# Optimization experiments

Hardware: AMD Instinct MI355X
Metric: run time of the kernel (lower is better)

## Reference

```python
import jax, jax.numpy as jnp
import numpy as np

N, E, H = 5000, 40000, 8
DIMS = [(258, 512), (516, 256), (262, 128), (136, 20)]  # (in_feature, out_feature) per GATDeformer


def setup_inputs() -> dict:
    key = jax.random.key(0)
    ks = jax.random.split(key, 10)
    s = 0.05
    data = jax.random.normal(ks[0], (N, 10), jnp.float32)
    src = jax.random.randint(ks[1], (E,), 0, N)
    off = jax.random.randint(ks[2], (E,), 1, N)
    edge_idx = jnp.stack([src, (src + off) % N]).astype(jnp.int32)  # no self loops by construction
    inp = {
        'data': data,
        'edge_idx': edge_idx,
        'W0': jax.random.normal(ks[3], (10, 256), jnp.float32) * s,
        'b0': jnp.zeros((256,), jnp.float32),
    }
    for i, (din, dout) in enumerate(DIMS, start=1):
        k = jax.random.split(ks[3 + i], 3)
        inp[f'W{i}'] = jax.random.normal(k[0], (din, H * dout), jnp.float32) * s
        inp[f'asrc{i}'] = jax.random.normal(k[1], (H, dout), jnp.float32) * s
        inp[f'adst{i}'] = jax.random.normal(k[2], (H, dout), jnp.float32) * s
        inp[f'bias{i}'] = jnp.zeros((dout,), jnp.float32)
    return inp


def _gat(x, src, dst, W, a_s, a_d, b):
    """PyG GATConv (concat=False): returns (mean-over-heads output + bias, alpha [E',H])."""
    Hh, C = a_s.shape
    h = (x @ W).reshape(N, Hh, C)                               # [N,H,C]
    e_s = jnp.einsum('nhc,hc->nh', h, a_s)                      # [N,H]
    e_d = jnp.einsum('nhc,hc->nh', h, a_d)
    logits = jax.nn.leaky_relu(e_s[src] + e_d[dst], 0.2)        # [E',H]
    m = jax.ops.segment_max(logits, dst, num_segments=N)        # segment softmax over incoming edges
    ex = jnp.exp(logits - m[dst])
    alpha = ex / jax.ops.segment_sum(ex, dst, num_segments=N)[dst]
    out = jax.ops.segment_sum(alpha[:, :, None] * h[src], dst, num_segments=N)  # [N,H,C]
    return out.mean(axis=1) + b, alpha


def _deformer(af, src, dst, W, a_s, a_d, b):
    # find_boundary on the layer input features
    up, down = af[:, 0] == 1.0, af[:, 0] == 0.0
    left, right = af[:, 1] == 0.0, af[:, 1] == 1.0
    feat, alpha = _gat(af, src, dst, W, a_s, a_d, b)
    coord = af[:, :2]
    # second propagate: alpha*0.2 reused to aggregate source coordinates, then mean over heads
    msg = (alpha * 0.2)[:, :, None] * coord[src][:, None, :]    # [E',H,2]
    oc = jax.ops.segment_sum(msg, dst, num_segments=N).mean(axis=1)
    # fix_boundary (sequential overwrite order: up then down, left then right)
    c0 = jnp.where(down, 0.0, jnp.where(up, 1.0, oc[:, 0]))
    c1 = jnp.where(right, 1.0, jnp.where(left, 0.0, oc[:, 1]))
    return jnp.stack([c0, c1], axis=1), jax.nn.selu(feat)


def reference(data, edge_idx, W0, b0, W1, asrc1, adst1, bias1, W2, asrc2, adst2, bias2, W3, asrc3, adst3, bias3, W4, asrc4, adst4, bias4):
    sl = jnp.arange(N, dtype=edge_idx.dtype)
    src = jnp.concatenate([edge_idx[0], sl])   # GATConv add_self_loops=True
    dst = jnp.concatenate([edge_idx[1], sl])
    coord = data[:, :2]
    feat = jax.nn.selu(data @ W0 + b0)
    c1_, f1 = _deformer(jnp.concatenate([coord, feat], 1), src, dst, W1, asrc1, adst1, bias1)
    c2_, f2 = _deformer(jnp.concatenate([c1_, coord, f1], 1), src, dst, W2, asrc2, adst2, bias2)
    c3_, f3 = _deformer(jnp.concatenate([c2_, c1_, coord, f2], 1), src, dst, W3, asrc3, adst3, bias3)
    c4_, _ = _deformer(jnp.concatenate([c3_, c2_, c1_, coord, f3], 1), src, dst, W4, asrc4, adst4, bias4)
    return c4_
```

## Files before the change

### kernel.cpp

```cpp
#include <hip/hip_runtime.h>

#define N_NODES 5000
#define NH 8

typedef unsigned short u16;
typedef short bf16x8 __attribute__((ext_vector_type(8)));
typedef float f32x4 __attribute__((ext_vector_type(4)));

static __device__ __forceinline__ float selu_f(float x) {
    const float sc = 1.0507009873554805f;
    const float al = 1.6732632423543772f;
    return x > 0.f ? sc * x : sc * al * (__expf(x) - 1.f);
}

static __device__ __forceinline__ u16 f2bf(float x) {
    union { float f; unsigned u; } v; v.f = x;
    unsigned r = v.u + 0x7fff + ((v.u >> 16) & 1);
    return (u16)(r >> 16);
}

static __device__ __forceinline__ float bf2f(unsigned hi16) {
    union { unsigned u; float f; } v; v.u = hi16 << 16;
    return v.f;
}

#define GL2LDS16(gp, lp)                                                        \
    __builtin_amdgcn_global_load_lds(                                           \
        (const __attribute__((address_space(1))) void*)(gp),                    \
        (__attribute__((address_space(3))) void*)(lp), 16, 0, 0)

__global__ void k_count(const int* __restrict__ ei, int* cnt, int E, int Esz) {
    int e = blockIdx.x * 256 + threadIdx.x;
    if (e >= Esz) return;
    int dst = (e < E) ? ei[E + e] : (e - E);
    atomicAdd(&cnt[dst], 1);
}

__global__ void k_scan(const int* __restrict__ cnt, int* __restrict__ rowp, int n) {
    __shared__ int ps[256];
    int t = threadIdx.x;
    int per = (n + 255) / 256;
    int b = t * per;
    int s = 0;
    for (int i = 0; i < per; ++i) { int idx = b + i; if (idx < n) s += cnt[idx]; }
    ps[t] = s;
    __syncthreads();
    for (int off = 1; off < 256; off <<= 1) {
        int v = (t >= off) ? ps[t - off] : 0;
        __syncthreads();
        ps[t] += v;
        __syncthreads();
    }
    int run = (t == 0) ? 0 : ps[t - 1];
    for (int i = 0; i < per; ++i) {
        int idx = b + i;
        if (idx < n) { rowp[idx] = run; run += cnt[idx]; }
    }
    if (t == 255) rowp[n] = run;
}

__global__ void k_fill(const int* __restrict__ ei, const int* __restrict__ rowp,
                       int* cur, int* ssrc, int E, int Esz) {
    int e = blockIdx.x * 256 + threadIdx.x;
    if (e >= Esz) return;
    int src, dst;
    if (e < E) { src = ei[e]; dst = ei[E + e]; }
    else       { src = e - E; dst = src; }
    int pos = rowp[dst] + atomicAdd(&cur[dst], 1);
    ssrc[pos] = src;
}

__global__ __launch_bounds__(256) void k_prep(
        const float* W1, const float* W2, const float* W3, const float* W4,
        const float* s1, const float* s2, const float* s3, const float* s4,
        const float* d1, const float* d2, const float* d3, const float* d4,
        float* __restrict__ fsAll, float* __restrict__ fdAll,
        u16* T1, u16* T2, u16* T3) {
    const int Ks[4] = {258, 516, 262, 136};
    const int Cs[4] = {512, 256, 128, 20};
    int bid = blockIdx.x;
    if (bid < 516) {
        int li = bid / 129;
        int k = (bid % 129) * 4 + (threadIdx.x >> 6);
        int lane = threadIdx.x & 63;
        if (k >= Ks[li]) return;
        const float* W  = (li == 0) ? W1 : (li == 1) ? W2 : (li == 2) ? W3 : W4;
        const float* as = (li == 0) ? s1 : (li == 1) ? s2 : (li == 2) ? s3 : s4;
        const float* ad = (li == 0) ? d1 : (li == 1) ? d2 : (li == 2) ? d3 : d4;
        int C = Cs[li];
        float s[8] = {0.f,0.f,0.f,0.f,0.f,0.f,0.f,0.f};
        float d[8] = {0.f,0.f,0.f,0.f,0.f,0.f,0.f,0.f};
        const float* wr = W + (size_t)k * 8 * C;
        for (int c = lane; c < C; c += 64) {
            #pragma unroll
            for (int h = 0; h < 8; ++h) {
                float w = wr[h * C + c];
                s[h] += w * as[h * C + c];
                d[h] += w * ad[h * C + c];
            }
        }
        #pragma unroll
        for (int off = 32; off >= 1; off >>= 1) {
            #pragma unroll
            for (int h = 0; h < 8; ++h) {
                s[h] += __shfl_xor(s[h], off);
                d[h] += __shfl_xor(d[h], off);
            }
        }
        if (lane == 0) {
            float* fo = fsAll + (size_t)li * 516 * 8 + k * 8;
            float* go = fdAll + (size_t)li * 516 * 8 + k * 8;
            #pragma unroll
            for (int h = 0; h < 8; ++h) { fo[h] = s[h]; go[h] = d[h]; }
        }
    } else {
        const int Kps[3] = {288, 544, 288};
        int w = bid - 516;
        int li = w / (16 * 136);
        int rem = w % (16 * 136);
        int c0 = (rem % 16) * 32;
        int j0 = (rem / 16) * 32;
        int C = Cs[li], K = Ks[li], Kp = Kps[li], KK = 8 * Kp;
        if (c0 >= C || j0 >= KK) return;
        const float* W = (li == 0) ? W1 : (li == 1) ? W2 : W3;
        u16* Wt2 = (li == 0) ? T1 : (li == 1) ? T2 : T3;
        __shared__ float tile[32][33];
        int h = j0 / Kp, k0 = j0 % Kp;
        int tid = threadIdx.x;
        for (int idx = tid; idx < 1024; idx += 256) {
            int kr = idx >> 5, cc = idx & 31;
            int gk = k0 + kr;
            tile[kr][cc] = (gk < K) ? W[(size_t)gk * (8 * C) + h * C + c0 + cc] : 0.f;
        }
        __syncthreads();
        for (int idx = tid; idx < 1024; idx += 256) {
            int cr = idx >> 5, kc = idx & 31;
            Wt2[(size_t)(c0 + cr) * KK + j0 + kc] = f2bf(tile[kc][cr]);
        }
    }
}

__global__ __launch_bounds__(256) void k_mf(const float* p0, const float* p1,
                                            const float* p2, const float* p3, int np,
                                            const float* __restrict__ data,
                                            const float* __restrict__ W0,
                                            const float* __restrict__ b0,
                                            const u16* __restrict__ facc,
                                            const float* __restrict__ biasp,
                                            int split, int MN, int FC, int K, int Kp,
                                            const float* __restrict__ fs,
                                            const float* __restrict__ fd,
                                            u16* __restrict__ afb,
                                            float* __restrict__ es, float* __restrict__ ed,
                                            float* __restrict__ c0out) {
    int n = blockIdx.x, t = threadIdx.x;
    __shared__ float drow[10];
    bool l1 = (biasp == nullptr);
    if (l1 && t < 10) drow[t] = data[n * 10 + t];
    __syncthreads();
    float pes[8] = {0.f,0.f,0.f,0.f,0.f,0.f,0.f,0.f};
    float ped[8] = {0.f,0.f,0.f,0.f,0.f,0.f,0.f,0.f};
    u16* rowb = afb + (size_t)n * Kp;
    for (int cf = t; cf < FC; cf += 256) {
        float v;
        if (l1) {
            v = b0[cf];
            #pragma unroll
            for (int k = 0; k < 10; ++k) v += drow[k] * W0[k * 256 + cf];
            v = selu_f(v);
        } else {
            float s = 0.f;
            for (int z = 0; z < split; ++z)
                s += bf2f(facc[(size_t)z * MN + (size_t)n * FC + cf]);
            v = selu_f(s * 0.125f + biasp[cf]);
        }
        int c = 2 * np + cf;
        rowb[c] = f2bf(v);
        const float* fsr = fs + c * 8;
        const float* fdr = fd + c * 8;
        #pragma unroll
        for (int h = 0; h < 8; ++h) { pes[h] += v * fsr[h]; ped[h] += v * fdr[h]; }
    }
    if (t < 2 * np) {
        float v;
        if (l1) {
            v = drow[t];
            c0out[n * 2 + t] = v;
        } else {
            const float* p = (t < 2) ? p0 : (t < 4) ? p1 : (t < 6) ? p2 : p3;
            v = p[n * 2 + (t & 1)];
        }
        rowb[t] = f2bf(v);
        #pragma unroll
        for (int h = 0; h < 8; ++h) { pes[h] += v * fs[t * 8 + h]; ped[h] += v * fd[t * 8 + h]; }
    }
    for (int c = K + t; c < Kp; c += 256) rowb[c] = 0;
    #pragma unroll
    for (int off = 32; off >= 1; off >>= 1) {
        #pragma unroll
        for (int h = 0; h < 8; ++h) {
            pes[h] += __shfl_xor(pes[h], off);
            ped[h] += __shfl_xor(ped[h], off);
        }
    }
    __shared__ float red[4][16];
    int wv = t >> 6, ln = t & 63;
    if (ln == 0) {
        #pragma unroll
        for (int h = 0; h < 8; ++h) { red[wv][h] = pes[h]; red[wv][8 + h] = ped[h]; }
    }
    __syncthreads();
    if (t < 16) {
        float s = red[0][t] + red[1][t] + red[2][t] + red[3][t];
        if (t < 8) es[n * 8 + t] = s;
        else       ed[n * 8 + (t - 8)] = s;
    }
}

template <int S32>
__global__ __launch_bounds__(256) void k_gag(const float* __restrict__ es,
                            const float* __restrict__ ed,
                            const int* __restrict__ rowp, const int* __restrict__ ssrc,
                            const float* __restrict__ cprev, const u16* __restrict__ afb,
                            u16* __restrict__ g, float* __restrict__ cnext, int Kp) {
    __shared__ int   ls[128];
    __shared__ float la[128 * 8];
    __shared__ float lc0[128], lc1[128], lw[128];
    __shared__ float linv[8];
    int n = blockIdx.x, t = threadIdx.x;
    int s0 = rowp[n];
    int deg = rowp[n + 1] - s0;
    if (deg > 128) deg = 128;
    for (int i = t; i < deg; i += 256) {
        int src = ssrc[s0 + i];
        ls[i] = src;
        lc0[i] = cprev[src * 2];
        lc1[i] = cprev[src * 2 + 1];
    }
    __syncthreads();
    for (int i = t; i < deg * 8; i += 256) {
        int e = i >> 3, h = i & 7;
        float x = es[ls[e] * 8 + h] + ed[n * 8 + h];
        la[i] = x > 0.f ? x : 0.2f * x;
    }
    __syncthreads();
    if (t < 8) {
        float m = -1e30f;
        for (int e = 0; e < deg; ++e) m = fmaxf(m, la[e * 8 + t]);
        float s = 0.f;
        for (int e = 0; e < deg; ++e) {
            float v = __expf(la[e * 8 + t] - m);
            la[e * 8 + t] = v;
            s += v;
        }
        linv[t] = 1.f / s;
    }
    __syncthreads();
    for (int i = t; i < deg; i += 256) {
        float w = 0.f;
        #pragma unroll
        for (int h = 0; h < 8; ++h) w += la[i * 8 + h] * linv[h];
        lw[i] = w;
    }
    int nW = Kp >> 1;
    float acc[8][2 * S32];
    #pragma unroll
    for (int h = 0; h < 8; ++h)
        #pragma unroll
        for (int s = 0; s < 2 * S32; ++s) acc[h][s] = 0.f;
    int e = 0;
    for (; e + 1 < deg; e += 2) {
        const unsigned* r0 = (const unsigned*)(afb + (size_t)ls[e] * Kp);
        const unsigned* r1 = (const unsigned*)(afb + (size_t)ls[e + 1] * Kp);
        unsigned v0[S32], v1[S32];
        #pragma unroll
        for (int s = 0; s < S32; ++s) {
            int w = t + 256 * s;
            v0[s] = (w < nW) ? r0[w] : 0u;
            v1[s] = (w < nW) ? r1[w] : 0u;
        }
        float a0[8], a1[8];
        #pragma unroll
        for (int h = 0; h < 8; ++h) { a0[h] = la[e * 8 + h]; a1[h] = la[(e + 1) * 8 + h]; }
        #pragma unroll
        for (int s = 0; s < S32; ++s) {
            float x0 = bf2f(v0[s] & 0xffff), y0 = bf2f(v0[s] >> 16);
            float x1 = bf2f(v1[s] & 0xffff), y1 = bf2f(v1[s] >> 16);
            #pragma unroll
            for (int h = 0; h < 8; ++h) {
                acc[h][2 * s]     += a0[h] * x0 + a1[h] * x1;
                acc[h][2 * s + 1] += a0[h] * y0 + a1[h] * y1;
            }
        }
    }
    if (e < deg) {
        const unsigned* r0 = (const unsigned*)(afb + (size_t)ls[e] * Kp);
        unsigned v0[S32];
        #pragma unroll
        for (int s = 0; s < S32; ++s) {
            int w = t + 256 * s;
            v0[s] = (w < nW) ? r0[w] : 0u;
        }
        float a0[8];
        #pragma unroll
        for (int h = 0; h < 8; ++h) a0[h] = la[e * 8 + h];
        #pragma unroll
        for (int s = 0; s < S32; ++s) {
            float x0 = bf2f(v0[s] & 0xffff), y0 = bf2f(v0[s] >> 16);
            #pragma unroll
            for (int h = 0; h < 8; ++h) {
                acc[h][2 * s]     += a0[h] * x0;
                acc[h][2 * s + 1] += a0[h] * y0;
            }
        }
    }
    unsigned* grw = (unsigned*)(g + (size_t)n * 8 * Kp);
    #pragma unroll
    for (int s = 0; s < S32; ++s) {
        int w = t + 256 * s;
        if (w < nW) {
            #pragma unroll
            for (int h = 0; h < 8; ++h) {
                float iv = linv[h];
                unsigned lo = f2bf(acc[h][2 * s] * iv);
                unsigned hi = f2bf(acc[h][2 * s + 1] * iv);
                grw[h * nW + w] = lo | (hi << 16);
            }
        }
    }
    __syncthreads();
    if (t == 0) {
        float oc0 = 0.f, oc1 = 0.f;
        for (int i = 0; i < deg; ++i) { oc0 += lw[i] * lc0[i]; oc1 += lw[i] * lc1[i]; }
        oc0 *= 0.025f; oc1 *= 0.025f;
        float a0 = cprev[n * 2], a1 = cprev[n * 2 + 1];
        cnext[n * 2]     = (a0 == 0.f) ? 0.f : ((a0 == 1.f) ? 1.f : oc0);
        cnext[n * 2 + 1] = (a1 == 1.f) ? 1.f : ((a1 == 0.f) ? 0.f : oc1);
    }
}

__global__ __launch_bounds__(256) void k_gemm_s(const u16* __restrict__ A,
                                                const u16* __restrict__ Bt,
                                                u16* __restrict__ facc16,
                                                int M, int KK, int NC, int kchunk, int MN) {
    __shared__ u16 As[128 * 32];
    __shared__ u16 Bs[128 * 32];
    int tid = threadIdx.x;
    int wave = tid >> 6, lane = tid & 63;
    int bm = blockIdx.y * 128, bn = blockIdx.x * 128, z = blockIdx.z;
    int kbeg = z * kchunk, kend = min(KK, kbeg + kchunk);
    int wm = (wave >> 1) * 64, wn = (wave & 1) * 64;
    int l16 = lane & 15, q = lane >> 4;
    f32x4 acc[4][4] = {};

    int seg0 = wave * 128 + lane;
    int seg1 = seg0 + 64;
    int row0 = seg0 >> 2, sq0 = (seg0 & 3) ^ (row0 & 3);
    int row1 = seg1 >> 2, sq1 = (seg1 & 3) ^ (row1 & 3);
    const u16* ga0 = A  + (size_t)(bm + row0) * KK + sq0 * 8;
    const u16* ga1 = A  + (size_t)(bm + row1) * KK + sq1 * 8;
    const u16* gb0 = Bt + (size_t)(bn + row0) * KK + sq0 * 8;
    const u16* gb1 = Bt + (size_t)(bn + row1) * KK + sq1 * 8;
    u16* lA0 = As + (wave * 2 + 0) * 512;
    u16* lA1 = As + (wave * 2 + 1) * 512;
    u16* lB0 = Bs + (wave * 2 + 0) * 512;
    u16* lB1 = Bs + (wave * 2 + 1) * 512;

    for (int k0 = kbeg; k0 < kend; k0 += 32) {
        GL2LDS16(ga0 + k0, lA0);
        GL2LDS16(ga1 + k0, lA1);
        GL2LDS16(gb0 + k0, lB0);
        GL2LDS16(gb1 + k0, lB1);
        __syncthreads();
        bf16x8 fa[4], fb[4];
        #pragma unroll
        for (int mi = 0; mi < 4; ++mi) {
            int row = wm + mi * 16 + l16;
            fa[mi] = *(const bf16x8*)(As + row * 32 + ((q ^ (row & 3)) * 8));
            int col = wn + mi * 16 + l16;
            fb[mi] = *(const bf16x8*)(Bs + col * 32 + ((q ^ (col & 3)) * 8));
        }
        #pragma unroll
        for (int mi = 0; mi < 4; ++mi)
            #pragma unroll
            for (int ni = 0; ni < 4; ++ni)
                acc[mi][ni] = __builtin_amdgcn_mfma_f32_16x16x32_bf16(fa[mi], fb[ni], acc[mi][ni], 0, 0, 0);
        __syncthreads();
    }
    u16* out = facc16 + (size_t)z * MN;
    #pragma unroll
    for (int mi = 0; mi < 4; ++mi) {
        int row0s = bm + wm + mi * 16 + q * 4;
        #pragma unroll
        for (int ni = 0; ni < 4; ++ni) {
            int col = bn + wn + ni * 16 + l16;
            #pragma unroll
            for (int r = 0; r < 4; ++r) {
                int row = row0s + r;
                if (row < M) out[(size_t)row * NC + col] = f2bf(acc[mi][ni][r]);
            }
        }
    }
}

__global__ void k_final(const float* __restrict__ es, const float* __restrict__ ed,
                        const int* __restrict__ rowp, const int* __restrict__ ssrc,
                        const float* __restrict__ cprev, float* __restrict__ outp) {
    int wid = (blockIdx.x * blockDim.x + threadIdx.x) >> 6;
    int lane = threadIdx.x & 63;
    if (wid >= N_NODES) return;
    int n = wid;
    int s0 = rowp[n], deg = rowp[n + 1] - s0;
    int h = lane & 7, ei = lane >> 3;
    float edh = ed[n * 8 + h];
    float m = -1e30f;
    for (int b = 0; b < deg; b += 8) {
        int e = b + ei;
        if (e < deg) {
            int src = ssrc[s0 + e];
            float x = es[src * 8 + h] + edh;
            x = x > 0.f ? x : 0.2f * x;
            m = fmaxf(m, x);
        }
    }
    m = fmaxf(m, __shfl_xor(m, 8));
    m = fmaxf(m, __shfl_xor(m, 16));
    m = fmaxf(m, __shfl_xor(m, 32));
    float ssum = 0.f;
    for (int b = 0; b < deg; b += 8) {
        int e = b + ei;
        if (e < deg) {
            int src = ssrc[s0 + e];
            float x = es[src * 8 + h] + edh;
            x = x > 0.f ? x : 0.2f * x;
            ssum += __expf(x - m);
        }
    }
    ssum += __shfl_xor(ssum, 8);
    ssum += __shfl_xor(ssum, 16);
    ssum += __shfl_xor(ssum, 32);
    float inv = 1.f / ssum;
    float oc0 = 0.f, oc1 = 0.f;
    for (int b = 0; b < deg; b += 8) {
        int e = b + ei;
        if (e < deg) {
            int src = ssrc[s0 + e];
            float x = es[src * 8 + h] + edh;
            x = x > 0.f ? x : 0.2f * x;
            float w = __expf(x - m) * inv;
            w += __shfl_xor(w, 1);
            w += __shfl_xor(w, 2);
            w += __shfl_xor(w, 4);
            if (h == 0) {
                oc0 += w * cprev[src * 2];
                oc1 += w * cprev[src * 2 + 1];
            }
        }
    }
    oc0 += __shfl_xor(oc0, 8);  oc1 += __shfl_xor(oc1, 8);
    oc0 += __shfl_xor(oc0, 16); oc1 += __shfl_xor(oc1, 16);
    oc0 += __shfl_xor(oc0, 32); oc1 += __shfl_xor(oc1, 32);
    if (lane == 0) {
        oc0 *= 0.025f; oc1 *= 0.025f;
        float a0 = cprev[n * 2], a1 = cprev[n * 2 + 1];
        outp[n * 2]     = (a0 == 0.f) ? 0.f : ((a0 == 1.f) ? 1.f : oc0);
        outp[n * 2 + 1] = (a1 == 1.f) ? 1.f : ((a1 == 0.f) ? 0.f : oc1);
    }
}

extern "C" void kernel_launch(void* const* d_in, const int* in_sizes, int n_in,
                              void* d_out, int out_size, void* d_ws, size_t ws_size,
                              hipStream_t stream) {
    const float* data = (const float*)d_in[0];
    const int* ei = (const int*)d_in[1];
    const float* W0 = (const float*)d_in[2];
    const float* b0 = (const float*)d_in[3];
    int E = in_sizes[1] / 2;
    int Esz = E + N_NODES;

    char* wp = (char*)d_ws;
    size_t off = 0;
    auto alloc = [&](size_t bytes) {
        void* p = wp + off;
        off += (bytes + 1023) & ~(size_t)1023;
        return p;
    };
    u16*   g     = (u16*)alloc((size_t)N_NODES * 8 * 576 * 2);
    u16*   T1    = (u16*)alloc((size_t)512 * 8 * 288 * 2);
    u16*   T2    = (u16*)alloc((size_t)256 * 8 * 544 * 2);
    u16*   T3    = (u16*)alloc((size_t)128 * 8 * 288 * 2);
    u16*   facc  = (u16*)alloc((size_t)8 * N_NODES * 512 * 2);
    u16*   afb   = (u16*)alloc((size_t)N_NODES * 576 * 2);
    float* es    = (float*)alloc((size_t)N_NODES * 8 * 4);
    float* ebd   = (float*)alloc((size_t)N_NODES * 8 * 4);
    float* fsAll = (float*)alloc((size_t)4 * 516 * 8 * 4);
    float* fdAll = (float*)alloc((size_t)4 * 516 * 8 * 4);
    float* c0    = (float*)alloc(N_NODES * 2 * 4);
    float* c1    = (float*)alloc(N_NODES * 2 * 4);
    float* c2    = (float*)alloc(N_NODES * 2 * 4);
    float* c3    = (float*)alloc(N_NODES * 2 * 4);
    int* cnt  = (int*)alloc(N_NODES * 2 * 4);
    int* cur  = cnt + N_NODES;
    int* rowp = (int*)alloc((N_NODES + 1) * 4);
    int* ssrc = (int*)alloc(Esz * 4);

    hipMemsetAsync(cnt, 0, N_NODES * 2 * 4, stream);
    int gE = (Esz + 255) / 256;
    k_count<<<gE, 256, 0, stream>>>(ei, cnt, E, Esz);
    k_scan<<<1, 256, 0, stream>>>(cnt, rowp, N_NODES);
    k_fill<<<gE, 256, 0, stream>>>(ei, rowp, cur, ssrc, E, Esz);

    struct LP { const float *W, *as, *ad, *bs; int K, C, split; };
    LP L[4] = {
        {(const float*)d_in[4],  (const float*)d_in[5],  (const float*)d_in[6],  (const float*)d_in[7],  258, 512, 4},
        {(const float*)d_in[8],  (const float*)d_in[9],  (const float*)d_in[10], (const float*)d_in[11], 516, 256, 8},
        {(const float*)d_in[12], (const float*)d_in[13], (const float*)d_in[14], (const float*)d_in[15], 262, 128, 8},
        {(const float*)d_in[16], (const float*)d_in[17], (const float*)d_in[18], (const float*)d_in[19], 136, 20, 1},
    };
    k_prep<<<516 + 16 * 136 * 3, 256, 0, stream>>>(
        L[0].W, L[1].W, L[2].W, L[3].W,
        L[0].as, L[1].as, L[2].as, L[3].as,
        L[0].ad, L[1].ad, L[2].ad, L[3].ad,
        fsAll, fdAll, T1, T2, T3);

    float* cbuf[4] = {c0, c1, c2, c3};
    u16* Tb[3] = {T1, T2, T3};
    int FC[4] = {256, 512, 256, 128};

    for (int li = 0; li < 4; ++li) {
        LP& lp = L[li];
        const float* p[4] = {nullptr, nullptr, nullptr, nullptr};
        for (int j = 0; j <= li; ++j) p[j] = cbuf[li - j];
        int Kp = ((lp.K + 31) / 32) * 32;
        int KK = 8 * Kp;
        const float* biasp = (li == 0) ? nullptr : L[li - 1].bs;
        int splitp = (li == 0) ? 1 : L[li - 1].split;
        int MNp = N_NODES * FC[li];
        const float* fs = fsAll + (size_t)li * 516 * 8;
        const float* fd = fdAll + (size_t)li * 516 * 8;

        k_mf<<<N_NODES, 256, 0, stream>>>(p[0], p[1], p[2], p[3], li + 1,
                                          data, W0, b0, facc, biasp, splitp, MNp, FC[li],
                                          lp.K, Kp, fs, fd, afb, es, ebd, c0);
        if (li < 3) {
            if ((Kp >> 1) <= 256)
                k_gag<1><<<N_NODES, 256, 0, stream>>>(es, ebd, rowp, ssrc, cbuf[li], afb,
                                                      g, cbuf[li + 1], Kp);
            else
                k_gag<2><<<N_NODES, 256, 0, stream>>>(es, ebd, rowp, ssrc, cbuf[li], afb,
                                                      g, cbuf[li + 1], Kp);
            int MN = N_NODES * lp.C;
            k_gemm_s<<<dim3(lp.C / 128, (N_NODES + 127) / 128, lp.split), 256, 0, stream>>>(
                g, Tb[li], facc, N_NODES, KK, lp.C, KK / lp.split, MN);
        } else {
            k_final<<<(N_NODES + 3) / 4, 256, 0, stream>>>(es, ebd, rowp, ssrc, cbuf[3],
                                                           (float*)d_out);
        }
    }
}
```

Before: 376.0 us.

## Double-buffer LDS tiles in split-K GEMM to overlap global loads with MFMA

The bf16 split-K GEMM now keeps two LDS buffers for the A and B tiles. It issues the direct global-to-LDS loads for the next K step before computing on the current one, and uses explicit vmcnt waits and raw s_barrier. This hides global load latency behind the MFMA work at the cost of twice the LDS per block, which may lower occupancy. Using s_barrier without an LDS waitcnt also leaves some risk around ordering the ds reads against the buffer being refilled.

Result: no change. 369.8 us (-1.7%).

```diff
diff --git a/kernel.cpp b/kernel.cpp
--- a/kernel.cpp
+++ b/kernel.cpp
@@ -343,8 +343,8 @@
                                                 const u16* __restrict__ Bt,
                                                 u16* __restrict__ facc16,
                                                 int M, int KK, int NC, int kchunk, int MN) {
-    __shared__ u16 As[128 * 32];
-    __shared__ u16 Bs[128 * 32];
+    __shared__ u16 As[2][128 * 32];
+    __shared__ u16 Bs[2][128 * 32];
     int tid = threadIdx.x;
     int wave = tid >> 6, lane = tid & 63;
     int bm = blockIdx.y * 128, bn = blockIdx.x * 128, z = blockIdx.z;
@@ -361,32 +361,46 @@
     const u16* ga1 = A  + (size_t)(bm + row1) * KK + sq1 * 8;
     const u16* gb0 = Bt + (size_t)(bn + row0) * KK + sq0 * 8;
     const u16* gb1 = Bt + (size_t)(bn + row1) * KK + sq1 * 8;
-    u16* lA0 = As + (wave * 2 + 0) * 512;
-    u16* lA1 = As + (wave * 2 + 1) * 512;
-    u16* lB0 = Bs + (wave * 2 + 0) * 512;
-    u16* lB1 = Bs + (wave * 2 + 1) * 512;
-
+    int lo0 = (wave * 2 + 0) * 512;
+    int lo1 = (wave * 2 + 1) * 512;
+
+#define STAGE_T(buf, kk)                          \
+    do {                                          \
+        GL2LDS16(ga0 + (kk), &As[buf][lo0]);      \
+        GL2LDS16(ga1 + (kk), &As[buf][lo1]);      \
+        GL2LDS16(gb0 + (kk), &Bs[buf][lo0]);      \
+        GL2LDS16(gb1 + (kk), &Bs[buf][lo1]);      \
+    } while (0)
+
+    STAGE_T(0, kbeg);
+    int cur = 0;
     for (int k0 = kbeg; k0 < kend; k0 += 32) {
-        GL2LDS16(ga0 + k0, lA0);
-        GL2LDS16(ga1 + k0, lA1);
-        GL2LDS16(gb0 + k0, lB0);
-        GL2LDS16(gb1 + k0, lB1);
-        __syncthreads();
+        if (k0 + 32 < kend) {
+            STAGE_T(cur ^ 1, k0 + 32);
+            asm volatile("s_waitcnt vmcnt(4)" ::: "memory");
+        } else {
+            asm volatile("s_waitcnt vmcnt(0)" ::: "memory");
+        }
+        __builtin_amdgcn_s_barrier();
+        const u16* Asr = As[cur];
+        const u16* Bsr = Bs[cur];
         bf16x8 fa[4], fb[4];
         #pragma unroll
         for (int mi = 0; mi < 4; ++mi) {
             int row = wm + mi * 16 + l16;
-            fa[mi] = *(const bf16x8*)(As + row * 32 + ((q ^ (row & 3)) * 8));
+            fa[mi] = *(const bf16x8*)(Asr + row * 32 + ((q ^ (row & 3)) * 8));
             int col = wn + mi * 16 + l16;
-            fb[mi] = *(const bf16x8*)(Bs + col * 32 + ((q ^ (col & 3)) * 8));
+            fb[mi] = *(const bf16x8*)(Bsr + col * 32 + ((q ^ (col & 3)) * 8));
         }
         #pragma unroll
         for (int mi = 0; mi < 4; ++mi)
             #pragma unroll
             for (int ni = 0; ni < 4; ++ni)
                 acc[mi][ni] = __builtin_amdgcn_mfma_f32_16x16x32_bf16(fa[mi], fb[ni], acc[mi][ni], 0, 0, 0);
-        __syncthreads();
-    }
+        __builtin_amdgcn_s_barrier();
+        cur ^= 1;
+    }
+#undef STAGE_T
     u16* out = facc16 + (size_t)z * MN;
     #pragma unroll
     for (int mi = 0; mi < 4; ++mi) {
```
